# Performance work log

Measured on AMD Instinct MI355X. Metric: run time of the kernel, lower is better.

Reference implementation:

```python
import jax, jax.numpy as jnp
import numpy as np
import math

W_BITS = 256.0  # default w_bits in forward()

def ste_round(x):
    # straight-through estimator round: identity gradient
    return x + jax.lax.stop_gradient(jnp.round(x) - x)

def setup_inputs() -> dict:
    key = jax.random.key(0)
    k1, k2 = jax.random.split(key)
    x_size, y_size = 4096, 4096
    xb = jax.random.normal(k1, (8192, x_size), dtype=jnp.float32)
    W = jax.random.normal(k2, (x_size, y_size), dtype=jnp.float32) / math.sqrt(x_size)
    b = jnp.zeros((y_size,), dtype=jnp.float32)
    return {"xb": xb, "W": W, "b": b}

def reference(xb, W, b):
    # train=True path: fake-quant the weights (per-tensor symmetric int8), then matmul + bias
    s_w = 2.0 * jnp.max(jnp.abs(W)) / W_BITS          # per-tensor scale (zero-point 0)
    w_q = jnp.clip(ste_round(W / s_w), -127.0, 127.0)  # quantize + clamp
    w_fq = s_w * w_q                                    # dequantize (fake-quant)
    return xb @ w_fq + b
```

## Files before the change

kernel.cpp:

```cpp
#include <hip/hip_runtime.h>
#include <hip/hip_bf16.h>
#include <stdint.h>

typedef unsigned short u16;
typedef unsigned int u32;
typedef __bf16 bf16x8 __attribute__((ext_vector_type(8)));
typedef float f32x4 __attribute__((ext_vector_type(4)));
typedef u16 u16x4 __attribute__((ext_vector_type(4)));
typedef u16 u16x8 __attribute__((ext_vector_type(8)));

typedef const __attribute__((address_space(1))) void* gas_ptr;
typedef __attribute__((address_space(3))) void* las_ptr;

#define M_DIM 8192
#define K_DIM 4096
#define N_DIM 4096

__device__ __forceinline__ u16 f32_to_bf16_rne(float f) {
    u32 u = __float_as_uint(f);
    u += 0x7FFFu + ((u >> 16) & 1u);
    return (u16)(u >> 16);
}

#define CAST_BLOCKS 4096
#define MAX_BLOCKS 1024
__global__ void cast_maxabs_kernel(const float* __restrict__ x, u16* __restrict__ y,
                                   const float* __restrict__ W, u32* __restrict__ out) {
    const int bid = blockIdx.x;
    if (bid < CAST_BLOCKS) {
        const int n4 = (M_DIM * K_DIM) / 4;
        int idx = bid * 256 + threadIdx.x;
        const int stride = CAST_BLOCKS * 256;
        const float4* x4 = (const float4*)x;
        u16x4* y4 = (u16x4*)y;
        for (int i = idx; i < n4; i += stride) {
            float4 v = x4[i];
            u16x4 o;
            o.x = f32_to_bf16_rne(v.x);
            o.y = f32_to_bf16_rne(v.y);
            o.z = f32_to_bf16_rne(v.z);
            o.w = f32_to_bf16_rne(v.w);
            y4[i] = o;
        }
    } else {
        const int n4 = (K_DIM * N_DIM) / 4;
        int idx = (bid - CAST_BLOCKS) * 256 + threadIdx.x;
        const int stride = MAX_BLOCKS * 256;
        const float4* W4 = (const float4*)W;
        float m = 0.0f;
        for (int i = idx; i < n4; i += stride) {
            float4 v = W4[i];
            m = fmaxf(m, fmaxf(fmaxf(fabsf(v.x), fabsf(v.y)), fmaxf(fabsf(v.z), fabsf(v.w))));
        }
#pragma unroll
        for (int off = 32; off > 0; off >>= 1)
            m = fmaxf(m, __shfl_down(m, off));
        if ((threadIdx.x & 63) == 0)
            atomicMax(out, __float_as_uint(m));
    }
}

__device__ __forceinline__ u16 quantize_bf16(float v, float s_inv) {
    float q = rintf(v * s_inv);
    q = fminf(fmaxf(q, -127.0f), 127.0f);
    return (u16)(__float_as_uint(q) >> 16);
}

__global__ void quant_transpose_kernel(const float* __restrict__ W, u16* __restrict__ Wt,
                                       const u32* __restrict__ mb) {
    __shared__ u16 tile[64][73];
    const float s_inv = 128.0f / __uint_as_float(*mb);
    const int n0 = blockIdx.x * 64;
    const int k0 = blockIdx.y * 64;
    const int t = threadIdx.x;

    const int lr = t >> 4;
    const int lc = (t & 15) * 4;
#pragma unroll
    for (int p = 0; p < 4; ++p) {
        const int k = k0 + p * 16 + lr;
        const float4 v = *(const float4*)&W[(size_t)k * N_DIM + n0 + lc];
        u16* d = &tile[p * 16 + lr][lc];
        d[0] = quantize_bf16(v.x, s_inv);
        d[1] = quantize_bf16(v.y, s_inv);
        d[2] = quantize_bf16(v.z, s_inv);
        d[3] = quantize_bf16(v.w, s_inv);
    }
    __syncthreads();

    const int sr = t >> 3;
    const int sc = (t & 7) * 8;
#pragma unroll
    for (int p = 0; p < 2; ++p) {
        const int n = p * 32 + sr;
        u16x8 o;
#pragma unroll
        for (int j = 0; j < 8; ++j) o[j] = tile[sc + j][n];
        *(u16x8*)&Wt[(size_t)(n0 + n) * K_DIM + k0 + sc] = o;
    }
}


#define BAR() __builtin_amdgcn_s_barrier()
#define SCB() __builtin_amdgcn_sched_barrier(0)
#define VMC(N) asm volatile("s_waitcnt vmcnt(" #N ")" ::: "memory")
#define PRIO1() __builtin_amdgcn_s_setprio(1)
#define PRIO0() __builtin_amdgcn_s_setprio(0)

#define DS_A(ABASE, MH)                                            \
    do {                                                           \
        _Pragma("unroll") for (int i_ = 0; i_ < 4; ++i_) {         \
            const char* p_ = (ABASE) + ((MH)*64 + i_ * 16) * 128;  \
            a[i_][0] = *(const bf16x8*)(p_ + ck0);                 \
            a[i_][1] = *(const bf16x8*)(p_ + ck1);                 \
        }                                                          \
    } while (0)

#define DS_B(BBASE, NH)                                            \
    do {                                                           \
        _Pragma("unroll") for (int j_ = 0; j_ < 2; ++j_) {         \
            const char* p_ = (BBASE) + ((NH)*32 + j_ * 16) * 128;  \
            b[(NH)*2 + j_][0] = *(const bf16x8*)(p_ + ck0);        \
            b[(NH)*2 + j_][1] = *(const bf16x8*)(p_ + ck1);        \
        }                                                          \
    } while (0)

#define MM(MH, NH)                                                                            \
    do {                                                                                      \
        _Pragma("unroll") for (int i_ = 0; i_ < 4; ++i_) {                                    \
            _Pragma("unroll") for (int j_ = 0; j_ < 2; ++j_) {                                \
                f32x4& c_ = acc[(MH)*4 + i_][(NH)*2 + j_];                                    \
                c_ = __builtin_amdgcn_mfma_f32_16x16x32_bf16(a[i_][0], b[(NH)*2 + j_][0], c_, \
                                                             0, 0, 0);                        \
                c_ = __builtin_amdgcn_mfma_f32_16x16x32_bf16(a[i_][1], b[(NH)*2 + j_][1], c_, \
                                                             0, 0, 0);                        \
            }                                                                                 \
        }                                                                                     \
    } while (0)

#define STAGE_A(BUF, T, HALF)                                                                 \
    do {                                                                                      \
        const int r0_ = wave * 8 + (HALF)*64;                                                 \
        const u16* s_ = Ag + (size_t)r0_ * K_DIM + (T)*64;                                    \
        __builtin_amdgcn_global_load_lds((gas_ptr)s_, (las_ptr)&lds[BUF][r0_ * 64], 16, 0,    \
                                         0);                                                  \
        __builtin_amdgcn_global_load_lds((gas_ptr)(s_ + (size_t)128 * K_DIM),                 \
                                         (las_ptr)&lds[BUF][(r0_ + 128) * 64], 16, 0, 0);     \
    } while (0)

#define STAGE_B(BUF, T, HALF)                                                                  \
    do {                                                                                       \
        const int r0_ = bw + (HALF)*32;                                                        \
        const u16* s_ = Bg + (size_t)r0_ * K_DIM + (T)*64;                                     \
        __builtin_amdgcn_global_load_lds((gas_ptr)s_, (las_ptr)&lds[2 + (BUF)][r0_ * 64], 16,  \
                                         0, 0);                                                \
        __builtin_amdgcn_global_load_lds((gas_ptr)(s_ + (size_t)128 * K_DIM),                  \
                                         (las_ptr)&lds[2 + (BUF)][(r0_ + 128) * 64], 16, 0,    \
                                         0);                                                   \
    } while (0)

#define KTILE(ABASE, BBASE, OBUF, TS)  \
    do {                               \
        VMC(2);                        \
        BAR();                         \
        SCB();                         \
        STAGE_A(OBUF, TS, 0);          \
        STAGE_B(OBUF, TS, 0);          \
        STAGE_B(OBUF, TS, 1);          \
        DS_A(ABASE, 0);                \
        DS_B(BBASE, 0);                \
        DS_B(BBASE, 1);                \
        SCB();                         \
        PRIO1();                       \
        MM(0, 0);                      \
        MM(0, 1);                      \
        PRIO0();                       \
        VMC(6);                        \
        BAR();                         \
        SCB();                         \
        STAGE_A(OBUF, TS, 1);          \
        DS_A(ABASE, 1);                \
        SCB();                         \
        PRIO1();                       \
        MM(1, 0);                      \
        MM(1, 1);                      \
        PRIO0();                       \
    } while (0)

__global__ __launch_bounds__(512, 2) void gemm_kernel(const u16* __restrict__ A,
                                                      const u16* __restrict__ Bt,
                                                      const float* __restrict__ bias,
                                                      const u32* __restrict__ mb,
                                                      float* __restrict__ out) {
    extern __shared__ u16 lds_raw[];
    u16(*lds)[256 * 64] = reinterpret_cast<u16(*)[256 * 64]>(lds_raw);

    const int tid = threadIdx.x;
    const int wave = tid >> 6;
    const int lane = tid & 63;
    const int quad = lane >> 4;
    const int l15 = lane & 15;
    const int wm = wave >> 2;
    const int wn = wave & 3;

    const int bswz = (blockIdx.x & 7) * 64 + (blockIdx.x >> 3);
    const int m0 = (bswz >> 4) * 256;
    const int n0 = (bswz & 15) * 256;

    const int stg_row = lane >> 3;
    const int stg_col = ((lane & 7) ^ stg_row) * 8;
    const u16* Ag = A + (size_t)(m0 + stg_row) * K_DIM + stg_col;
    const u16* Bg = Bt + (size_t)(n0 + stg_row) * K_DIM + stg_col;
    const int bw = (wave & 3) * 8 + (wave >> 2) * 64;

    const int xorv = (l15 & 7) << 4;
    const int ck0 = (quad * 16) ^ xorv;
    const int ck1 = (64 + quad * 16) ^ xorv;

    const char* asb0 = (const char*)&lds[0][0] + wm * 16384 + l15 * 128;
    const char* asb1 = asb0 + 32768;
    const char* bsb0 = (const char*)&lds[2][0] + wn * 8192 + l15 * 128;
    const char* bsb1 = bsb0 + 32768;

    bf16x8 a[4][2];
    bf16x8 b[4][2];
    f32x4 acc[8][4];
#pragma unroll
    for (int i = 0; i < 8; i++)
#pragma unroll
        for (int j = 0; j < 4; j++) acc[i][j] = (f32x4){0.f, 0.f, 0.f, 0.f};

    STAGE_A(0, 0, 0);
    STAGE_B(0, 0, 0);
    STAGE_B(0, 0, 1);
    STAGE_A(0, 0, 1);

#pragma unroll 1
    for (int t = 0; t < 64; t += 2) {
        KTILE(asb0, bsb0, 1, t + 1);
        KTILE(asb1, bsb1, 0, (t + 2) & 63);
    }
    VMC(0);

    const float s_w = __uint_as_float(*mb) * (1.0f / 128.0f);
#pragma unroll
    for (int nj = 0; nj < 4; ++nj) {
        const int col = n0 + wn * 64 + nj * 16 + l15;
        const float bv = bias[col];
#pragma unroll
        for (int mi = 0; mi < 8; ++mi) {
            const int row = m0 + wm * 128 + mi * 16 + quad * 4;
            float* op = out + (size_t)row * N_DIM + col;
#pragma unroll
            for (int r = 0; r < 4; ++r) op[(size_t)r * N_DIM] = s_w * acc[mi][nj][r] + bv;
        }
    }
}

extern "C" void kernel_launch(void* const* d_in, const int* in_sizes, int n_in,
                              void* d_out, int out_size, void* d_ws, size_t ws_size,
                              hipStream_t stream) {
    const float* xb = (const float*)d_in[0];
    const float* W = (const float*)d_in[1];
    const float* b = (const float*)d_in[2];
    float* out = (float*)d_out;

    u32* mb = (u32*)d_ws;
    u16* xb_bf = (u16*)((char*)d_ws + 256);
    u16* wqt = (u16*)((char*)d_ws + 256 + (size_t)M_DIM * K_DIM * 2);

    hipMemsetAsync(d_ws, 0, 4, stream);
    cast_maxabs_kernel<<<CAST_BLOCKS + MAX_BLOCKS, 256, 0, stream>>>(xb, xb_bf, W, mb);
    quant_transpose_kernel<<<dim3(N_DIM / 64, K_DIM / 64), 256, 0, stream>>>(W, wqt, mb);
    gemm_kernel<<<dim3(512), dim3(512), 131072, stream>>>(xb_bf, wqt, b, mb, out);
}
```

Measured before the change: 527.4 us.

## Pre-swizzle quantized weights into MFMA fragment layout and load B directly to registers

Measured after the change: 570.8 us. 8.2% more time.

```diff
diff --git a/kernel.cpp b/kernel.cpp
--- a/kernel.cpp
+++ b/kernel.cpp
@@ -90,118 +90,112 @@
 
     const int sr = t >> 3;
     const int sc = (t & 7) * 8;
+    const int j = (sr >> 4) & 1;
+    const int l15 = sr & 15;
+    const int ks = sc >> 5;
+    const int quad = (sc >> 3) & 3;
+    const size_t base = ((size_t)blockIdx.x * 64 + blockIdx.y) * 4096;
 #pragma unroll
     for (int p = 0; p < 2; ++p) {
-        const int n = p * 32 + sr;
         u16x8 o;
 #pragma unroll
-        for (int j = 0; j < 8; ++j) o[j] = tile[sc + j][n];
-        *(u16x8*)&Wt[(size_t)(n0 + n) * K_DIM + k0 + sc] = o;
+        for (int e = 0; e < 8; ++e) o[e] = tile[sc + e][p * 32 + sr];
+        const size_t off = base + (size_t)(((p * 2 + j) * 2 + ks) * 512 + (quad * 16 + l15) * 8);
+        *(u16x8*)&Wt[off] = o;
     }
 }
 
 
 #define BAR() __builtin_amdgcn_s_barrier()
 #define SCB() __builtin_amdgcn_sched_barrier(0)
-#define VMC(N) asm volatile("s_waitcnt vmcnt(" #N ")" ::: "memory")
+#define LGKM0()                                            \
+    do {                                                   \
+        asm volatile("s_waitcnt lgkmcnt(0)" ::: "memory"); \
+        __builtin_amdgcn_sched_barrier(0);                 \
+    } while (0)
+#define VMC(N)                                                  \
+    do {                                                        \
+        asm volatile("s_waitcnt vmcnt(" #N ")" ::: "memory");   \
+        __builtin_amdgcn_sched_barrier(0);                      \
+    } while (0)
 #define PRIO1() __builtin_amdgcn_s_setprio(1)
 #define PRIO0() __builtin_amdgcn_s_setprio(0)
 
-#define DS_A(ABASE, MH)                                            \
-    do {                                                           \
-        _Pragma("unroll") for (int i_ = 0; i_ < 4; ++i_) {         \
-            const char* p_ = (ABASE) + ((MH)*64 + i_ * 16) * 128;  \
-            a[i_][0] = *(const bf16x8*)(p_ + ck0);                 \
-            a[i_][1] = *(const bf16x8*)(p_ + ck1);                 \
-        }                                                          \
-    } while (0)
-
-#define DS_B(BBASE, NH)                                            \
-    do {                                                           \
-        _Pragma("unroll") for (int j_ = 0; j_ < 2; ++j_) {         \
-            const char* p_ = (BBASE) + ((NH)*32 + j_ * 16) * 128;  \
-            b[(NH)*2 + j_][0] = *(const bf16x8*)(p_ + ck0);        \
-            b[(NH)*2 + j_][1] = *(const bf16x8*)(p_ + ck1);        \
-        }                                                          \
-    } while (0)
-
-#define MM(MH, NH)                                                                            \
-    do {                                                                                      \
-        _Pragma("unroll") for (int i_ = 0; i_ < 4; ++i_) {                                    \
-            _Pragma("unroll") for (int j_ = 0; j_ < 2; ++j_) {                                \
-                f32x4& c_ = acc[(MH)*4 + i_][(NH)*2 + j_];                                    \
-                c_ = __builtin_amdgcn_mfma_f32_16x16x32_bf16(a[i_][0], b[(NH)*2 + j_][0], c_, \
-                                                             0, 0, 0);                        \
-                c_ = __builtin_amdgcn_mfma_f32_16x16x32_bf16(a[i_][1], b[(NH)*2 + j_][1], c_, \
-                                                             0, 0, 0);                        \
-            }                                                                                 \
-        }                                                                                     \
-    } while (0)
-
-#define STAGE_A(BUF, T, HALF)                                                                 \
-    do {                                                                                      \
-        const int r0_ = wave * 8 + (HALF)*64;                                                 \
-        const u16* s_ = Ag + (size_t)r0_ * K_DIM + (T)*64;                                    \
-        __builtin_amdgcn_global_load_lds((gas_ptr)s_, (las_ptr)&lds[BUF][r0_ * 64], 16, 0,    \
-                                         0);                                                  \
-        __builtin_amdgcn_global_load_lds((gas_ptr)(s_ + (size_t)128 * K_DIM),                 \
-                                         (las_ptr)&lds[BUF][(r0_ + 128) * 64], 16, 0, 0);     \
-    } while (0)
-
-#define STAGE_B(BUF, T, HALF)                                                                  \
+#define DS_ALL(BUFOFF)                                          \
+    do {                                                        \
+        _Pragma("unroll") for (int mi_ = 0; mi_ < 8; ++mi_) {   \
+            const char* p_ = asb + (BUFOFF) + mi_ * 2048;       \
+            a[mi_][0] = *(const bf16x8*)(p_ + ck0);             \
+            a[mi_][1] = *(const bf16x8*)(p_ + ck1);             \
+        }                                                       \
+    } while (0)
+
+#define LOADB(T, C) \
+    b[(C) >> 1][(C)&1] = *(const bf16x8*)(Bw + (size_t)(T)*4096 + (C)*512 + lane * 8)
+
+#define CL(NH)                                                                                  \
+    do {                                                                                        \
+        _Pragma("unroll") for (int mi_ = 0; mi_ < 8; ++mi_) {                                   \
+            _Pragma("unroll") for (int j_ = 0; j_ < 2; ++j_) {                                  \
+                f32x4& c_ = acc[mi_][(NH)*2 + j_];                                              \
+                c_ = __builtin_amdgcn_mfma_f32_16x16x32_bf16(a[mi_][0], b[(NH)*2 + j_][0], c_,  \
+                                                             0, 0, 0);                          \
+                c_ = __builtin_amdgcn_mfma_f32_16x16x32_bf16(a[mi_][1], b[(NH)*2 + j_][1], c_,  \
+                                                             0, 0, 0);                          \
+            }                                                                                   \
+        }                                                                                       \
+    } while (0)
+
+#define STAGE_A4(BUFOFF, T)                                                                    \
     do {                                                                                       \
-        const int r0_ = bw + (HALF)*32;                                                        \
-        const u16* s_ = Bg + (size_t)r0_ * K_DIM + (T)*64;                                     \
-        __builtin_amdgcn_global_load_lds((gas_ptr)s_, (las_ptr)&lds[2 + (BUF)][r0_ * 64], 16,  \
-                                         0, 0);                                                \
-        __builtin_amdgcn_global_load_lds((gas_ptr)(s_ + (size_t)128 * K_DIM),                  \
-                                         (las_ptr)&lds[2 + (BUF)][(r0_ + 128) * 64], 16, 0,    \
-                                         0);                                                   \
-    } while (0)
-
-#define KTILE(ABASE, BBASE, OBUF, TS)  \
-    do {                               \
-        VMC(2);                        \
-        BAR();                         \
-        SCB();                         \
-        STAGE_A(OBUF, TS, 0);          \
-        STAGE_B(OBUF, TS, 0);          \
-        STAGE_B(OBUF, TS, 1);          \
-        DS_A(ABASE, 0);                \
-        DS_B(BBASE, 0);                \
-        DS_B(BBASE, 1);                \
-        SCB();                         \
-        PRIO1();                       \
-        MM(0, 0);                      \
-        MM(0, 1);                      \
-        PRIO0();                       \
-        VMC(6);                        \
-        BAR();                         \
-        SCB();                         \
-        STAGE_A(OBUF, TS, 1);          \
-        DS_A(ABASE, 1);                \
-        SCB();                         \
-        PRIO1();                       \
-        MM(1, 0);                      \
-        MM(1, 1);                      \
-        PRIO0();                       \
+        _Pragma("unroll") for (int h_ = 0; h_ < 4; ++h_) {                                     \
+            const int r0_ = wave_u * 8 + h_ * 64;                                              \
+            __builtin_amdgcn_global_load_lds((gas_ptr)(Ag + (size_t)r0_ * K_DIM + (T)*64),     \
+                                             (las_ptr)(lds_raw + (BUFOFF) + r0_ * 128), 16, 0, \
+                                             0);                                               \
+        }                                                                                      \
+    } while (0)
+
+#define KTILE(BUFOFF, OBUFOFF, T)     \
+    do {                              \
+        LOADB(T, 4);                  \
+        LOADB(T, 5);                  \
+        LOADB(T, 6);                  \
+        LOADB(T, 7);                  \
+        STAGE_A4(OBUFOFF, (T) + 1);   \
+        DS_ALL(BUFOFF);               \
+        LGKM0();                      \
+        VMC(8);                       \
+        PRIO1();                      \
+        CL(0);                        \
+        PRIO0();                      \
+        LOADB((T) + 1, 0);            \
+        LOADB((T) + 1, 1);            \
+        LOADB((T) + 1, 2);            \
+        LOADB((T) + 1, 3);            \
+        VMC(8);                       \
+        PRIO1();                      \
+        CL(1);                        \
+        PRIO0();                      \
+        VMC(4);                       \
+        BAR();                        \
     } while (0)
 
 __global__ __launch_bounds__(512, 2) void gemm_kernel(const u16* __restrict__ A,
-                                                      const u16* __restrict__ Bt,
+                                                      const u16* __restrict__ Btt,
                                                       const float* __restrict__ bias,
                                                       const u32* __restrict__ mb,
                                                       float* __restrict__ out) {
-    extern __shared__ u16 lds_raw[];
-    u16(*lds)[256 * 64] = reinterpret_cast<u16(*)[256 * 64]>(lds_raw);
+    extern __shared__ u16 lds_u16[];
+    char* lds_raw = (char*)lds_u16;
 
     const int tid = threadIdx.x;
-    const int wave = tid >> 6;
+    const int wave_u = __builtin_amdgcn_readfirstlane(tid >> 6);
     const int lane = tid & 63;
     const int quad = lane >> 4;
     const int l15 = lane & 15;
-    const int wm = wave >> 2;
-    const int wn = wave & 3;
+    const int wm = wave_u >> 2;
+    const int wn = wave_u & 3;
 
     const int bswz = (blockIdx.x & 7) * 64 + (blockIdx.x >> 3);
     const int m0 = (bswz >> 4) * 256;
@@ -210,19 +204,15 @@
     const int stg_row = lane >> 3;
     const int stg_col = ((lane & 7) ^ stg_row) * 8;
     const u16* Ag = A + (size_t)(m0 + stg_row) * K_DIM + stg_col;
-    const u16* Bg = Bt + (size_t)(n0 + stg_row) * K_DIM + stg_col;
-    const int bw = (wave & 3) * 8 + (wave >> 2) * 64;
+
+    const u16* Bw = Btt + (size_t)((n0 >> 6) + wn) * 262144;
 
     const int xorv = (l15 & 7) << 4;
     const int ck0 = (quad * 16) ^ xorv;
     const int ck1 = (64 + quad * 16) ^ xorv;
-
-    const char* asb0 = (const char*)&lds[0][0] + wm * 16384 + l15 * 128;
-    const char* asb1 = asb0 + 32768;
-    const char* bsb0 = (const char*)&lds[2][0] + wn * 8192 + l15 * 128;
-    const char* bsb1 = bsb0 + 32768;
-
-    bf16x8 a[4][2];
+    const char* asb = lds_raw + wm * 16384 + l15 * 128;
+
+    bf16x8 a[8][2];
     bf16x8 b[4][2];
     f32x4 acc[8][4];
 #pragma unroll
@@ -230,17 +220,34 @@
 #pragma unroll
         for (int j = 0; j < 4; j++) acc[i][j] = (f32x4){0.f, 0.f, 0.f, 0.f};
 
-    STAGE_A(0, 0, 0);
-    STAGE_B(0, 0, 0);
-    STAGE_B(0, 0, 1);
-    STAGE_A(0, 0, 1);
+    STAGE_A4(0, 0);
+    LOADB(0, 0);
+    LOADB(0, 1);
+    LOADB(0, 2);
+    LOADB(0, 3);
+    VMC(4);
+    BAR();
 
 #pragma unroll 1
-    for (int t = 0; t < 64; t += 2) {
-        KTILE(asb0, bsb0, 1, t + 1);
-        KTILE(asb1, bsb1, 0, (t + 2) & 63);
-    }
+    for (int t = 0; t < 62; t += 2) {
+        KTILE(0, 32768, t);
+        KTILE(32768, 0, t + 1);
+    }
+    KTILE(0, 32768, 62);
+    LOADB(63, 4);
+    LOADB(63, 5);
+    LOADB(63, 6);
+    LOADB(63, 7);
+    DS_ALL(32768);
+    LGKM0();
+    VMC(4);
+    PRIO1();
+    CL(0);
+    PRIO0();
     VMC(0);
+    PRIO1();
+    CL(1);
+    PRIO0();
 
     const float s_w = __uint_as_float(*mb) * (1.0f / 128.0f);
 #pragma unroll
@@ -272,5 +279,5 @@
     hipMemsetAsync(d_ws, 0, 4, stream);
     cast_maxabs_kernel<<<CAST_BLOCKS + MAX_BLOCKS, 256, 0, stream>>>(xb, xb_bf, W, mb);
     quant_transpose_kernel<<<dim3(N_DIM / 64, K_DIM / 64), 256, 0, stream>>>(W, wqt, mb);
-    gemm_kernel<<<dim3(512), dim3(512), 131072, stream>>>(xb_bf, wqt, b, mb, out);
-}
+    gemm_kernel<<<dim3(512), dim3(512), 65536, stream>>>(xb_bf, wqt, b, mb, out);
+}
```
